# Kernel tuning notes

Measured on AMD Instinct MI355X. Metric: run time of the kernel, lower is better.

The kernel has to match this reference:

```python
import jax, jax.numpy as jnp
import numpy as np

TEMPERATURE = 0.1

def _l2norm(x):
    # F.normalize(dim=1) with eps clamp
    n = jnp.maximum(jnp.linalg.norm(x, axis=1, keepdims=True), 1e-12)
    return x / n

def _retrieval_metric(s):
    # T=1: position of the diagonal element in each row's descending sort.
    order = jnp.argsort(-s, axis=1)            # [N,N] descending argsort
    rankpos = jnp.argsort(order, axis=1)        # inverse permutation: rank of each column
    pos = jnp.diagonal(rankpos)                 # j such that rank[i][j] == i
    posf = pos.astype(s.dtype)
    r1 = jnp.mean((pos < 1).astype(s.dtype))
    r5 = jnp.mean((pos < 5).astype(s.dtype))
    r10 = jnp.mean((pos < 10).astype(s.dtype))
    mr = jnp.mean(posf)
    return r1, r5, r10, mr

def setup_inputs() -> dict:
    key = jax.random.key(0)
    k1, k2, k3, k4 = jax.random.split(key, 4)
    N, C = 4096, 512
    return {
        'v_feat': jax.random.normal(k1, (N, C), dtype=jnp.float32),
        't_feat': jax.random.normal(k2, (N, C), dtype=jnp.float32),
        'p_v': jax.random.normal(k3, (N, C), dtype=jnp.float32),
        'p_t': jax.random.normal(k4, (N, C), dtype=jnp.float32),
    }

def reference(v_feat, t_feat, p_v, p_t):
    vn = _l2norm(v_feat)
    tn = _l2norm(t_feat)
    pvn = _l2norm(p_v)
    ptn = _l2norm(p_t)
    sv = jnp.einsum('nc,mc->nm', vn, ptn) / TEMPERATURE  # [N,N]
    st = jnp.einsum('nc,mc->nm', tn, pvn) / TEMPERATURE  # [N,N]
    # nominator: scalar logsumexp over both diagonals (2N values)
    nominator = jax.nn.logsumexp(jnp.concatenate([jnp.diagonal(sv), jnp.diagonal(st)], axis=0))
    # denominator: per-row logsumexp over concatenated [N,2N]
    denominator = jax.nn.logsumexp(jnp.concatenate([sv, st], axis=1), axis=1)
    loss = jnp.mean(denominator - nominator)
    # metrics (no-grad path in original)
    v_std = jnp.mean(jnp.std(vn, axis=0, ddof=1))
    t_std = jnp.mean(jnp.std(tn, axis=0, ddof=1))
    pv_std = jnp.mean(jnp.std(pvn, axis=0, ddof=1))
    pt_std = jnp.mean(jnp.std(ptn, axis=0, ddof=1))
    sv_raw = jnp.einsum('nc,mc->nm', vn, ptn)
    st_raw = jnp.einsum('nc,mc->nm', tn, pvn)
    v_r1, v_r5, v_r10, v_mr = _retrieval_metric(sv_raw)
    t_r1, t_r5, t_r10, t_mr = _retrieval_metric(st_raw)
    return (loss, v_std, t_std, pv_std, pt_std,
            v_r1, v_r5, v_r10, v_mr,
            t_r1, t_r5, t_r10, t_mr)
```

## Files before the change

### kernel.cpp

```cpp
#include <hip/hip_runtime.h>
#include <hip/hip_bf16.h>

#define N 4096
#define C 512

typedef __attribute__((ext_vector_type(8))) short bf16x8;
typedef __attribute__((ext_vector_type(8))) short s16x8;
typedef __attribute__((ext_vector_type(4))) float f32x4;

__device__ inline float bf2f(__hip_bfloat16 h) { return __bfloat162float(h); }
__device__ inline float bfbits2f(unsigned short b) {
    union { unsigned u; float f; } c; c.u = ((unsigned)b) << 16; return c.f;
}

__device__ inline void gload16(const void* g, void* l) {
    __builtin_amdgcn_global_load_lds(
        (__attribute__((address_space(1))) void*)(g),
        (__attribute__((address_space(3))) void*)(l),
        16, 0, 0);
}

__global__ __launch_bounds__(256) void k_norm_split(
    const float* __restrict__ s0, const float* __restrict__ s1f,
    const float* __restrict__ s2f, const float* __restrict__ s3,
    __hip_bfloat16* __restrict__ ws_hi0, long mat_stride)
{
    const int m = blockIdx.x >> 12;
    const int row = blockIdx.x & 4095;
    const int tid = threadIdx.x;
    const float* src = (m == 0) ? s0 : (m == 1) ? s1f : (m == 2) ? s2f : s3;
    __hip_bfloat16* hi = ws_hi0 + (long)m * mat_stride;
    __hip_bfloat16* lo = hi + (long)N * C;

    const float2* r = (const float2*)(src + (size_t)row * C);
    float2 x = r[tid];
    float ss = x.x * x.x + x.y * x.y;
    for (int o = 1; o < 64; o <<= 1) ss += __shfl_xor(ss, o);
    __shared__ float wsum[4];
    if ((tid & 63) == 0) wsum[tid >> 6] = ss;
    __syncthreads();
    float tot = wsum[0] + wsum[1] + wsum[2] + wsum[3];
    float scale = 1.0f / fmaxf(sqrtf(tot), 1e-12f);
    float y0 = x.x * scale, y1 = x.y * scale;
    __hip_bfloat16 h0 = __float2bfloat16(y0);
    __hip_bfloat16 h1 = __float2bfloat16(y1);
    __hip_bfloat16 l0 = __float2bfloat16(y0 - bf2f(h0));
    __hip_bfloat16 l1 = __float2bfloat16(y1 - bf2f(h1));
    size_t base = (size_t)row * C + 2 * tid;
    hi[base] = h0; hi[base + 1] = h1;
    lo[base] = l0; lo[base + 1] = l1;
}

__global__ __launch_bounds__(256) void k_diag(
    const unsigned short* __restrict__ h0, const unsigned short* __restrict__ l0,
    const unsigned short* __restrict__ h1, const unsigned short* __restrict__ l1,
    const unsigned short* __restrict__ h2, const unsigned short* __restrict__ l2,
    const unsigned short* __restrict__ h3, const unsigned short* __restrict__ l3,
    float* __restrict__ dv, float* __restrict__ dt)
{
    const int lane = threadIdx.x & 63;
    const int w = threadIdx.x >> 6;
    const int row = blockIdx.x * 4 + w;
    const int z = blockIdx.y;
    const unsigned short* ah = z ? h1 : h0;
    const unsigned short* al = z ? l1 : l0;
    const unsigned short* bh = z ? h2 : h3;
    const unsigned short* bl = z ? l2 : l3;
    float* dout = z ? dt : dv;

    size_t base = (size_t)row * C + lane * 8;
    s16x8 xh = *(const s16x8*)(ah + base);
    s16x8 xl = *(const s16x8*)(al + base);
    s16x8 yh = *(const s16x8*)(bh + base);
    s16x8 yl = *(const s16x8*)(bl + base);
    float s = 0.f;
    for (int e = 0; e < 8; e++) {
        float a = bfbits2f((unsigned short)xh[e]);
        float b = bfbits2f((unsigned short)xl[e]);
        float c = bfbits2f((unsigned short)yh[e]);
        float d = bfbits2f((unsigned short)yl[e]);
        s += a * c + a * d + b * c;
    }
    for (int o = 1; o < 64; o <<= 1) s += __shfl_xor(s, o);
    if (lane == 0) dout[row] = s;
}

__global__ __launch_bounds__(256) void k_gemm(
    const __hip_bfloat16* __restrict__ h0, const __hip_bfloat16* __restrict__ l0,
    const __hip_bfloat16* __restrict__ h1, const __hip_bfloat16* __restrict__ l1,
    const __hip_bfloat16* __restrict__ h2, const __hip_bfloat16* __restrict__ l2,
    const __hip_bfloat16* __restrict__ h3, const __hip_bfloat16* __restrict__ l3,
    const float* __restrict__ dv, const float* __restrict__ dt,
    float* __restrict__ pev, float* __restrict__ pet,
    float* __restrict__ pcv, float* __restrict__ pct)
{
    __shared__ __align__(16) __hip_bfloat16 sA[2][128][32];
    __shared__ __align__(16) __hip_bfloat16 sB[2][128][32];
    __shared__ float sdiag[128];
    __shared__ float sred[128][2][2];

    const int z = blockIdx.z;
    const __hip_bfloat16* Ah = z ? h1 : h0;
    const __hip_bfloat16* Al = z ? l1 : l0;
    const __hip_bfloat16* Bh = z ? h2 : h3;
    const __hip_bfloat16* Bl = z ? l2 : l3;
    const float* diag = z ? dt : dv;
    float* pe = z ? pet : pev;
    float* pc = z ? pct : pcv;

    const int tid = threadIdx.x;
    const int lane = tid & 63;
    const int w = tid >> 6;
    const int wy = w >> 1, wx = w & 1;
    const int bm = blockIdx.x * 128;
    const int bn = blockIdx.y * 128;

    if (tid < 128) sdiag[tid] = diag[bm + tid];

    f32x4 acc[4][4];
    for (int i = 0; i < 4; i++)
        for (int j = 0; j < 4; j++)
            acc[i][j] = (f32x4){0.f, 0.f, 0.f, 0.f};

    const int srow = lane >> 2;
    const int scol = (lane & 3) * 8;
    const int fr = lane & 15;
    const int fq = (lane >> 4) * 8;

    for (int k0 = 0; k0 < C; k0 += 32) {
        for (int half = 0; half < 2; half++) {
            int rr = w * 16 + half * 64 + srow;
            size_t ga = (size_t)(bm + rr) * C + k0 + scol;
            size_t gb = (size_t)(bn + rr) * C + k0 + scol;
            gload16(Ah + ga, &sA[0][rr][scol]);
            gload16(Al + ga, &sA[1][rr][scol]);
            gload16(Bh + gb, &sB[0][rr][scol]);
            gload16(Bl + gb, &sB[1][rr][scol]);
        }
        __syncthreads();

        bf16x8 a_h[4], a_l[4], b_h[4], b_l[4];
        for (int i = 0; i < 4; i++) {
            a_h[i] = *(const bf16x8*)&sA[0][wy * 64 + i * 16 + fr][fq];
            a_l[i] = *(const bf16x8*)&sA[1][wy * 64 + i * 16 + fr][fq];
            b_h[i] = *(const bf16x8*)&sB[0][wx * 64 + i * 16 + fr][fq];
            b_l[i] = *(const bf16x8*)&sB[1][wx * 64 + i * 16 + fr][fq];
        }
        for (int i = 0; i < 4; i++)
            for (int j = 0; j < 4; j++) {
                acc[i][j] = __builtin_amdgcn_mfma_f32_16x16x32_bf16(a_h[i], b_h[j], acc[i][j], 0, 0, 0);
                acc[i][j] = __builtin_amdgcn_mfma_f32_16x16x32_bf16(a_h[i], b_l[j], acc[i][j], 0, 0, 0);
                acc[i][j] = __builtin_amdgcn_mfma_f32_16x16x32_bf16(a_l[i], b_h[j], acc[i][j], 0, 0, 0);
            }
        __syncthreads();
    }

    const int quad = lane >> 4;
    for (int i = 0; i < 4; i++) {
        for (int reg = 0; reg < 4; reg++) {
            int rloc = wy * 64 + i * 16 + quad * 4 + reg;
            int grow = bm + rloc;
            float d = sdiag[rloc];
            float e = 0.f, c = 0.f;
            for (int j = 0; j < 4; j++) {
                float s = acc[i][j][reg];
                int gcol = bn + wx * 64 + j * 16 + fr;
                e += __expf(10.f * s - 10.f);
                if (s > d && gcol != grow) c += 1.f;
            }
            for (int o = 1; o < 16; o <<= 1) {
                e += __shfl_xor(e, o);
                c += __shfl_xor(c, o);
            }
            if (fr == 0) { sred[rloc][wx][0] = e; sred[rloc][wx][1] = c; }
        }
    }
    __syncthreads();
    if (tid < 128) {
        size_t idx = (size_t)(bm + tid) * 32 + blockIdx.y;
        pe[idx] = sred[tid][0][0] + sred[tid][1][0];
        pc[idx] = sred[tid][0][1] + sred[tid][1][1];
    }
}

__global__ __launch_bounds__(512) void k_stdp(
    const __hip_bfloat16* __restrict__ ws_hi0, long mat_stride,
    float* __restrict__ s1, float* __restrict__ s2)
{
    const int col = threadIdx.x;
    const int chunk = blockIdx.x;
    const int m = blockIdx.y;
    const __hip_bfloat16* hi = ws_hi0 + (long)m * mat_stride;
    const __hip_bfloat16* lo = hi + (long)N * C;
    float a = 0.f, b = 0.f;
    for (int r = chunk * 64; r < chunk * 64 + 64; r++) {
        float y = bf2f(hi[(size_t)r * C + col]) + bf2f(lo[(size_t)r * C + col]);
        a += y;
        b += y * y;
    }
    size_t idx = ((size_t)m * 64 + chunk) * 512 + col;
    s1[idx] = a;
    s2[idx] = b;
}

__global__ __launch_bounds__(64) void k_rowred(
    const float* __restrict__ dv, const float* __restrict__ dt,
    const float* __restrict__ pev, const float* __restrict__ pet,
    const float* __restrict__ pcv, const float* __restrict__ pct,
    float* __restrict__ partials)
{
    const int lane = threadIdx.x;
    const int row = blockIdx.x * 64 + lane;

    float se = 0.f, pv = 0.f, pt = 0.f;
    for (int cb = 0; cb < 32; cb++) {
        se += pev[(size_t)row * 32 + cb] + pet[(size_t)row * 32 + cb];
        pv += pcv[(size_t)row * 32 + cb];
        pt += pct[(size_t)row * 32 + cb];
    }

    float vals[10];
    vals[0] = logf(se) + 10.f;
    vals[1] = (pv < 0.5f) ? 1.f : 0.f;
    vals[2] = (pv < 4.5f) ? 1.f : 0.f;
    vals[3] = (pv < 9.5f) ? 1.f : 0.f;
    vals[4] = pv;
    vals[5] = (pt < 0.5f) ? 1.f : 0.f;
    vals[6] = (pt < 4.5f) ? 1.f : 0.f;
    vals[7] = (pt < 9.5f) ? 1.f : 0.f;
    vals[8] = pt;
    vals[9] = __expf(10.f * dv[row] - 10.f) + __expf(10.f * dt[row] - 10.f);

    for (int k = 0; k < 10; k++) {
        float v = vals[k];
        for (int o = 1; o < 64; o <<= 1) v += __shfl_xor(v, o);
        if (lane == k) partials[(size_t)blockIdx.x * 10 + k] = v;
    }
}

__global__ __launch_bounds__(64) void k_colstd(
    const float* __restrict__ s1, const float* __restrict__ s2,
    float* __restrict__ stdpart)
{
    const int lane = threadIdx.x;
    const int m = blockIdx.x >> 3;
    const int col = (blockIdx.x & 7) * 64 + lane;
    float a = 0.f, b = 0.f;
    for (int ch = 0; ch < 64; ch++) {
        size_t idx = ((size_t)m * 64 + ch) * 512 + col;
        a += s1[idx];
        b += s2[idx];
    }
    float var = (b - a * a * (1.f / N)) * (1.f / (N - 1));
    float sd = sqrtf(fmaxf(var, 0.f));
    for (int o = 1; o < 64; o <<= 1) sd += __shfl_xor(sd, o);
    if (lane == 0) stdpart[blockIdx.x] = sd;
}

__global__ __launch_bounds__(64) void k_final2(
    const float* __restrict__ partials,
    const float* __restrict__ stdpart,
    float* __restrict__ out)
{
    const int lane = threadIdx.x;
    float v = 0.f;
    if (lane < 10) {
        for (int b = 0; b < 64; b++) v += partials[b * 10 + lane];
    }
    __shared__ float g[10];
    __shared__ float stds[4];
    if (lane < 10) g[lane] = v;
    if (lane < 4) {
        float s = 0.f;
        for (int i = 0; i < 8; i++) s += stdpart[lane * 8 + i];
        stds[lane] = s * (1.f / 512.f);
    }
    __syncthreads();
    if (lane == 0) {
        const float invN = 1.f / N;
        float nominator = logf(g[9]) + 10.f;
        out[0]  = g[0] * invN - nominator;
        out[1]  = stds[0];
        out[2]  = stds[1];
        out[3]  = stds[2];
        out[4]  = stds[3];
        out[5]  = g[1] * invN;
        out[6]  = g[2] * invN;
        out[7]  = g[3] * invN;
        out[8]  = g[4] * invN;
        out[9]  = g[5] * invN;
        out[10] = g[6] * invN;
        out[11] = g[7] * invN;
        out[12] = g[8] * invN;
    }
}

extern "C" void kernel_launch(void* const* d_in, const int* in_sizes, int n_in,
                              void* d_out, int out_size, void* d_ws, size_t ws_size,
                              hipStream_t stream)
{
    char* p = (char*)d_ws;
    const size_t NE = (size_t)N * C;
    const long mat_stride = 2 * NE;
    __hip_bfloat16* hiA[4];
    __hip_bfloat16* loA[4];
    for (int m = 0; m < 4; m++) {
        hiA[m] = (__hip_bfloat16*)p; p += NE * 2;
        loA[m] = (__hip_bfloat16*)p; p += NE * 2;
    }
    float* dv  = (float*)p; p += N * 4;
    float* dt  = (float*)p; p += N * 4;
    float* pev = (float*)p; p += 32 * N * 4;
    float* pet = (float*)p; p += 32 * N * 4;
    float* pcv = (float*)p; p += 32 * N * 4;
    float* pct = (float*)p; p += 32 * N * 4;
    float* s1  = (float*)p; p += 4 * 64 * 512 * 4;
    float* s2  = (float*)p; p += 4 * 64 * 512 * 4;
    float* partials = (float*)p; p += 64 * 10 * 4;
    float* stdpart  = (float*)p; p += 32 * 4;

    k_norm_split<<<dim3(4 * N), 256, 0, stream>>>(
        (const float*)d_in[0], (const float*)d_in[1],
        (const float*)d_in[2], (const float*)d_in[3],
        hiA[0], mat_stride);

    k_diag<<<dim3(N / 4, 2), 256, 0, stream>>>(
        (const unsigned short*)hiA[0], (const unsigned short*)loA[0],
        (const unsigned short*)hiA[1], (const unsigned short*)loA[1],
        (const unsigned short*)hiA[2], (const unsigned short*)loA[2],
        (const unsigned short*)hiA[3], (const unsigned short*)loA[3],
        dv, dt);

    k_gemm<<<dim3(32, 32, 2), 256, 0, stream>>>(
        hiA[0], loA[0], hiA[1], loA[1], hiA[2], loA[2], hiA[3], loA[3],
        dv, dt, pev, pet, pcv, pct);

    k_stdp<<<dim3(64, 4), 512, 0, stream>>>(hiA[0], mat_stride, s1, s2);

    k_rowred<<<dim3(64), 64, 0, stream>>>(dv, dt, pev, pet, pcv, pct, partials);
    k_colstd<<<dim3(32), 64, 0, stream>>>(s1, s2, stdpart);
    k_final2<<<dim3(1), 64, 0, stream>>>(partials, stdpart, (float*)d_out);
}
```

Baseline: 223.5 us.

## Fuse prep kernels, swizzle GEMM LDS layout, merge final reductions via atomic counter

Merges normalization/split, diagonal dot products, and column std statistics into one k_prep launch. Diagonals and column sums are now computed directly from the fp32 inputs, so the bf16 hi/lo buffers are no longer re-read. The GEMM staging gains an XOR swizzle on LDS columns to reduce bank conflicts on fragment reads. The three tail kernels collapse into one k_fin that uses a last-block atomic counter for the final combine. This cuts launch count and memory traffic, at the cost of heavier prep blocks and reliance on threadfence/atomic ordering.

```diff
diff --git a/kernel.cpp b/kernel.cpp
--- a/kernel.cpp
+++ b/kernel.cpp
@@ -20,69 +20,109 @@
         16, 0, 0);
 }
 
-__global__ __launch_bounds__(256) void k_norm_split(
+__global__ __launch_bounds__(256) void k_prep(
     const float* __restrict__ s0, const float* __restrict__ s1f,
     const float* __restrict__ s2f, const float* __restrict__ s3,
-    __hip_bfloat16* __restrict__ ws_hi0, long mat_stride)
+    __hip_bfloat16* __restrict__ ws_hi0, long mat_stride,
+    float* __restrict__ dv, float* __restrict__ dt,
+    float* __restrict__ st1, float* __restrict__ st2,
+    unsigned int* __restrict__ counter)
 {
-    const int m = blockIdx.x >> 12;
-    const int row = blockIdx.x & 4095;
+    __shared__ float sa[4][512];
+    __shared__ float sb[4][512];
+
+    const int b = blockIdx.x;
     const int tid = threadIdx.x;
-    const float* src = (m == 0) ? s0 : (m == 1) ? s1f : (m == 2) ? s2f : s3;
-    __hip_bfloat16* hi = ws_hi0 + (long)m * mat_stride;
-    __hip_bfloat16* lo = hi + (long)N * C;
-
-    const float2* r = (const float2*)(src + (size_t)row * C);
-    float2 x = r[tid];
-    float ss = x.x * x.x + x.y * x.y;
-    for (int o = 1; o < 64; o <<= 1) ss += __shfl_xor(ss, o);
-    __shared__ float wsum[4];
-    if ((tid & 63) == 0) wsum[tid >> 6] = ss;
-    __syncthreads();
-    float tot = wsum[0] + wsum[1] + wsum[2] + wsum[3];
-    float scale = 1.0f / fmaxf(sqrtf(tot), 1e-12f);
-    float y0 = x.x * scale, y1 = x.y * scale;
-    __hip_bfloat16 h0 = __float2bfloat16(y0);
-    __hip_bfloat16 h1 = __float2bfloat16(y1);
-    __hip_bfloat16 l0 = __float2bfloat16(y0 - bf2f(h0));
-    __hip_bfloat16 l1 = __float2bfloat16(y1 - bf2f(h1));
-    size_t base = (size_t)row * C + 2 * tid;
-    hi[base] = h0; hi[base + 1] = h1;
-    lo[base] = l0; lo[base + 1] = l1;
-}
-
-__global__ __launch_bounds__(256) void k_diag(
-    const unsigned short* __restrict__ h0, const unsigned short* __restrict__ l0,
-    const unsigned short* __restrict__ h1, const unsigned short* __restrict__ l1,
-    const unsigned short* __restrict__ h2, const unsigned short* __restrict__ l2,
-    const unsigned short* __restrict__ h3, const unsigned short* __restrict__ l3,
-    float* __restrict__ dv, float* __restrict__ dt)
-{
-    const int lane = threadIdx.x & 63;
-    const int w = threadIdx.x >> 6;
-    const int row = blockIdx.x * 4 + w;
-    const int z = blockIdx.y;
-    const unsigned short* ah = z ? h1 : h0;
-    const unsigned short* al = z ? l1 : l0;
-    const unsigned short* bh = z ? h2 : h3;
-    const unsigned short* bl = z ? l2 : l3;
-    float* dout = z ? dt : dv;
-
-    size_t base = (size_t)row * C + lane * 8;
-    s16x8 xh = *(const s16x8*)(ah + base);
-    s16x8 xl = *(const s16x8*)(al + base);
-    s16x8 yh = *(const s16x8*)(bh + base);
-    s16x8 yl = *(const s16x8*)(bl + base);
-    float s = 0.f;
-    for (int e = 0; e < 8; e++) {
-        float a = bfbits2f((unsigned short)xh[e]);
-        float b = bfbits2f((unsigned short)xl[e]);
-        float c = bfbits2f((unsigned short)yh[e]);
-        float d = bfbits2f((unsigned short)yl[e]);
-        s += a * c + a * d + b * c;
-    }
-    for (int o = 1; o < 64; o <<= 1) s += __shfl_xor(s, o);
-    if (lane == 0) dout[row] = s;
+    const int lane = tid & 63;
+    const int w = tid >> 6;
+
+    if (b == 0 && tid == 0) *counter = 0;
+
+    if (b < 4096) {
+        const int grow = b * 4 + w;
+        const int m = grow >> 12;
+        const int row = grow & 4095;
+        const float* src = (m == 0) ? s0 : (m == 1) ? s1f : (m == 2) ? s2f : s3;
+        __hip_bfloat16* hi = ws_hi0 + (long)m * mat_stride;
+        __hip_bfloat16* lo = hi + (long)N * C;
+
+        const float4* r4 = (const float4*)(src + (size_t)row * C);
+        float4 x0 = r4[lane * 2];
+        float4 x1 = r4[lane * 2 + 1];
+        float ss = x0.x*x0.x + x0.y*x0.y + x0.z*x0.z + x0.w*x0.w
+                 + x1.x*x1.x + x1.y*x1.y + x1.z*x1.z + x1.w*x1.w;
+        for (int o = 1; o < 64; o <<= 1) ss += __shfl_xor(ss, o);
+        float scale = 1.0f / fmaxf(sqrtf(ss), 1e-12f);
+        float y[8] = { x0.x*scale, x0.y*scale, x0.z*scale, x0.w*scale,
+                       x1.x*scale, x1.y*scale, x1.z*scale, x1.w*scale };
+        __hip_bfloat16 hv[8], lv[8];
+        for (int e = 0; e < 8; e++) {
+            hv[e] = __float2bfloat16(y[e]);
+            lv[e] = __float2bfloat16(y[e] - bf2f(hv[e]));
+        }
+        size_t base = (size_t)row * C + lane * 8;
+        *(s16x8*)(hi + base) = *(s16x8*)hv;
+        *(s16x8*)(lo + base) = *(s16x8*)lv;
+    } else if (b < 6144) {
+        const int idx = b - 4096;
+        const int z = idx >> 10;
+        const int row = (idx & 1023) * 4 + w;
+        const float* A = z ? s1f : s0;
+        const float* B = z ? s2f : s3;
+        float* dout = z ? dt : dv;
+
+        const float4* a4 = (const float4*)(A + (size_t)row * C);
+        const float4* b4 = (const float4*)(B + (size_t)row * C);
+        float4 a0 = a4[lane * 2], a1 = a4[lane * 2 + 1];
+        float4 b0 = b4[lane * 2], b1 = b4[lane * 2 + 1];
+        float ssa = a0.x*a0.x + a0.y*a0.y + a0.z*a0.z + a0.w*a0.w
+                  + a1.x*a1.x + a1.y*a1.y + a1.z*a1.z + a1.w*a1.w;
+        float ssb = b0.x*b0.x + b0.y*b0.y + b0.z*b0.z + b0.w*b0.w
+                  + b1.x*b1.x + b1.y*b1.y + b1.z*b1.z + b1.w*b1.w;
+        float dot = a0.x*b0.x + a0.y*b0.y + a0.z*b0.z + a0.w*b0.w
+                  + a1.x*b1.x + a1.y*b1.y + a1.z*b1.z + a1.w*b1.w;
+        for (int o = 1; o < 64; o <<= 1) {
+            ssa += __shfl_xor(ssa, o);
+            ssb += __shfl_xor(ssb, o);
+            dot += __shfl_xor(dot, o);
+        }
+        if (lane == 0)
+            dout[row] = dot / (fmaxf(sqrtf(ssa), 1e-12f) * fmaxf(sqrtf(ssb), 1e-12f));
+    } else {
+        const int idx = b - 6144;
+        const int m = idx >> 5;
+        const int chunk = idx & 31;
+        const float* src = (m == 0) ? s0 : (m == 1) ? s1f : (m == 2) ? s2f : s3;
+        const int slice = w;
+
+        float a[8], q[8];
+        for (int e = 0; e < 8; e++) { a[e] = 0.f; q[e] = 0.f; }
+        const int row0 = chunk * 128 + slice * 32;
+        for (int r = 0; r < 32; r++) {
+            const float4* r4 = (const float4*)(src + (size_t)(row0 + r) * C);
+            float4 x0 = r4[lane * 2];
+            float4 x1 = r4[lane * 2 + 1];
+            float ss = x0.x*x0.x + x0.y*x0.y + x0.z*x0.z + x0.w*x0.w
+                     + x1.x*x1.x + x1.y*x1.y + x1.z*x1.z + x1.w*x1.w;
+            for (int o = 1; o < 64; o <<= 1) ss += __shfl_xor(ss, o);
+            float scale = 1.0f / fmaxf(sqrtf(ss), 1e-12f);
+            float y[8] = { x0.x*scale, x0.y*scale, x0.z*scale, x0.w*scale,
+                           x1.x*scale, x1.y*scale, x1.z*scale, x1.w*scale };
+            for (int e = 0; e < 8; e++) { a[e] += y[e]; q[e] += y[e] * y[e]; }
+        }
+        for (int e = 0; e < 8; e++) {
+            sa[slice][lane * 8 + e] = a[e];
+            sb[slice][lane * 8 + e] = q[e];
+        }
+        __syncthreads();
+        for (int c = tid; c < 512; c += 256) {
+            float A = sa[0][c] + sa[1][c] + sa[2][c] + sa[3][c];
+            float B = sb[0][c] + sb[1][c] + sb[2][c] + sb[3][c];
+            size_t o = ((size_t)m * 32 + chunk) * 512 + c;
+            st1[o] = A;
+            st2[o] = B;
+        }
+    }
 }
 
 __global__ __launch_bounds__(256) void k_gemm(
@@ -123,28 +163,29 @@
             acc[i][j] = (f32x4){0.f, 0.f, 0.f, 0.f};
 
     const int srow = lane >> 2;
-    const int scol = (lane & 3) * 8;
+    const int lcol = (lane & 3) * 8;
+    const int scolg = (((lane & 3) ^ ((lane >> 3) & 3))) * 8;
     const int fr = lane & 15;
-    const int fq = (lane >> 4) * 8;
+    const int pcs = ((lane >> 4) ^ ((fr >> 1) & 3)) * 8;
 
     for (int k0 = 0; k0 < C; k0 += 32) {
         for (int half = 0; half < 2; half++) {
             int rr = w * 16 + half * 64 + srow;
-            size_t ga = (size_t)(bm + rr) * C + k0 + scol;
-            size_t gb = (size_t)(bn + rr) * C + k0 + scol;
-            gload16(Ah + ga, &sA[0][rr][scol]);
-            gload16(Al + ga, &sA[1][rr][scol]);
-            gload16(Bh + gb, &sB[0][rr][scol]);
-            gload16(Bl + gb, &sB[1][rr][scol]);
+            size_t ga = (size_t)(bm + rr) * C + k0 + scolg;
+            size_t gb = (size_t)(bn + rr) * C + k0 + scolg;
+            gload16(Ah + ga, &sA[0][rr][lcol]);
+            gload16(Al + ga, &sA[1][rr][lcol]);
+            gload16(Bh + gb, &sB[0][rr][lcol]);
+            gload16(Bl + gb, &sB[1][rr][lcol]);
         }
         __syncthreads();
 
         bf16x8 a_h[4], a_l[4], b_h[4], b_l[4];
         for (int i = 0; i < 4; i++) {
-            a_h[i] = *(const bf16x8*)&sA[0][wy * 64 + i * 16 + fr][fq];
-            a_l[i] = *(const bf16x8*)&sA[1][wy * 64 + i * 16 + fr][fq];
-            b_h[i] = *(const bf16x8*)&sB[0][wx * 64 + i * 16 + fr][fq];
-            b_l[i] = *(const bf16x8*)&sB[1][wx * 64 + i * 16 + fr][fq];
+            a_h[i] = *(const bf16x8*)&sA[0][wy * 64 + i * 16 + fr][pcs];
+            a_l[i] = *(const bf16x8*)&sA[1][wy * 64 + i * 16 + fr][pcs];
+            b_h[i] = *(const bf16x8*)&sB[0][wx * 64 + i * 16 + fr][pcs];
+            b_l[i] = *(const bf16x8*)&sB[1][wx * 64 + i * 16 + fr][pcs];
         }
         for (int i = 0; i < 4; i++)
             for (int j = 0; j < 4; j++) {
@@ -183,89 +224,75 @@
     }
 }
 
-__global__ __launch_bounds__(512) void k_stdp(
-    const __hip_bfloat16* __restrict__ ws_hi0, long mat_stride,
-    float* __restrict__ s1, float* __restrict__ s2)
-{
-    const int col = threadIdx.x;
-    const int chunk = blockIdx.x;
-    const int m = blockIdx.y;
-    const __hip_bfloat16* hi = ws_hi0 + (long)m * mat_stride;
-    const __hip_bfloat16* lo = hi + (long)N * C;
-    float a = 0.f, b = 0.f;
-    for (int r = chunk * 64; r < chunk * 64 + 64; r++) {
-        float y = bf2f(hi[(size_t)r * C + col]) + bf2f(lo[(size_t)r * C + col]);
-        a += y;
-        b += y * y;
-    }
-    size_t idx = ((size_t)m * 64 + chunk) * 512 + col;
-    s1[idx] = a;
-    s2[idx] = b;
-}
-
-__global__ __launch_bounds__(64) void k_rowred(
+__global__ __launch_bounds__(64) void k_fin(
     const float* __restrict__ dv, const float* __restrict__ dt,
     const float* __restrict__ pev, const float* __restrict__ pet,
     const float* __restrict__ pcv, const float* __restrict__ pct,
-    float* __restrict__ partials)
+    const float* __restrict__ st1, const float* __restrict__ st2,
+    float* __restrict__ partials, float* __restrict__ stdpart,
+    unsigned int* __restrict__ counter, float* __restrict__ out)
 {
+    const int b = blockIdx.x;
     const int lane = threadIdx.x;
-    const int row = blockIdx.x * 64 + lane;
-
-    float se = 0.f, pv = 0.f, pt = 0.f;
-    for (int cb = 0; cb < 32; cb++) {
-        se += pev[(size_t)row * 32 + cb] + pet[(size_t)row * 32 + cb];
-        pv += pcv[(size_t)row * 32 + cb];
-        pt += pct[(size_t)row * 32 + cb];
-    }
-
-    float vals[10];
-    vals[0] = logf(se) + 10.f;
-    vals[1] = (pv < 0.5f) ? 1.f : 0.f;
-    vals[2] = (pv < 4.5f) ? 1.f : 0.f;
-    vals[3] = (pv < 9.5f) ? 1.f : 0.f;
-    vals[4] = pv;
-    vals[5] = (pt < 0.5f) ? 1.f : 0.f;
-    vals[6] = (pt < 4.5f) ? 1.f : 0.f;
-    vals[7] = (pt < 9.5f) ? 1.f : 0.f;
-    vals[8] = pt;
-    vals[9] = __expf(10.f * dv[row] - 10.f) + __expf(10.f * dt[row] - 10.f);
-
-    for (int k = 0; k < 10; k++) {
-        float v = vals[k];
-        for (int o = 1; o < 64; o <<= 1) v += __shfl_xor(v, o);
-        if (lane == k) partials[(size_t)blockIdx.x * 10 + k] = v;
-    }
-}
-
-__global__ __launch_bounds__(64) void k_colstd(
-    const float* __restrict__ s1, const float* __restrict__ s2,
-    float* __restrict__ stdpart)
-{
-    const int lane = threadIdx.x;
-    const int m = blockIdx.x >> 3;
-    const int col = (blockIdx.x & 7) * 64 + lane;
-    float a = 0.f, b = 0.f;
-    for (int ch = 0; ch < 64; ch++) {
-        size_t idx = ((size_t)m * 64 + ch) * 512 + col;
-        a += s1[idx];
-        b += s2[idx];
-    }
-    float var = (b - a * a * (1.f / N)) * (1.f / (N - 1));
-    float sd = sqrtf(fmaxf(var, 0.f));
-    for (int o = 1; o < 64; o <<= 1) sd += __shfl_xor(sd, o);
-    if (lane == 0) stdpart[blockIdx.x] = sd;
-}
-
-__global__ __launch_bounds__(64) void k_final2(
-    const float* __restrict__ partials,
-    const float* __restrict__ stdpart,
-    float* __restrict__ out)
-{
-    const int lane = threadIdx.x;
+
+    if (b < 64) {
+        const int row = b * 64 + lane;
+        float se = 0.f, pv = 0.f, pt = 0.f;
+        const float4* e4v = (const float4*)(pev + (size_t)row * 32);
+        const float4* e4t = (const float4*)(pet + (size_t)row * 32);
+        const float4* c4v = (const float4*)(pcv + (size_t)row * 32);
+        const float4* c4t = (const float4*)(pct + (size_t)row * 32);
+        for (int q = 0; q < 8; q++) {
+            float4 a = e4v[q], bb = e4t[q], c = c4v[q], d = c4t[q];
+            se += a.x + a.y + a.z + a.w + bb.x + bb.y + bb.z + bb.w;
+            pv += c.x + c.y + c.z + c.w;
+            pt += d.x + d.y + d.z + d.w;
+        }
+        float vals[10];
+        vals[0] = logf(se) + 10.f;
+        vals[1] = (pv < 0.5f) ? 1.f : 0.f;
+        vals[2] = (pv < 4.5f) ? 1.f : 0.f;
+        vals[3] = (pv < 9.5f) ? 1.f : 0.f;
+        vals[4] = pv;
+        vals[5] = (pt < 0.5f) ? 1.f : 0.f;
+        vals[6] = (pt < 4.5f) ? 1.f : 0.f;
+        vals[7] = (pt < 9.5f) ? 1.f : 0.f;
+        vals[8] = pt;
+        vals[9] = __expf(10.f * dv[row] - 10.f) + __expf(10.f * dt[row] - 10.f);
+        for (int k = 0; k < 10; k++) {
+            float v = vals[k];
+            for (int o = 1; o < 64; o <<= 1) v += __shfl_xor(v, o);
+            if (lane == k) partials[(size_t)b * 10 + k] = v;
+        }
+    } else {
+        const int idx = b - 64;
+        const int m = idx >> 3;
+        const int col = (idx & 7) * 64 + lane;
+        float a = 0.f, q = 0.f;
+        for (int ch = 0; ch < 32; ch++) {
+            size_t o = ((size_t)m * 32 + ch) * 512 + col;
+            a += st1[o];
+            q += st2[o];
+        }
+        float var = (q - a * a * (1.f / N)) * (1.f / (N - 1));
+        float sd = sqrtf(fmaxf(var, 0.f));
+        for (int o = 1; o < 64; o <<= 1) sd += __shfl_xor(sd, o);
+        if (lane == 0) stdpart[idx] = sd;
+    }
+
+    __syncthreads();
+    __shared__ unsigned int s_old;
+    if (lane == 0) {
+        __threadfence();
+        s_old = atomicAdd(counter, 1u);
+    }
+    __syncthreads();
+    if (s_old != 95) return;
+    __threadfence();
+
     float v = 0.f;
     if (lane < 10) {
-        for (int b = 0; b < 64; b++) v += partials[b * 10 + lane];
+        for (int k = 0; k < 64; k++) v += partials[k * 10 + lane];
     }
     __shared__ float g[10];
     __shared__ float stds[4];
@@ -314,30 +341,22 @@
     float* pet = (float*)p; p += 32 * N * 4;
     float* pcv = (float*)p; p += 32 * N * 4;
     float* pct = (float*)p; p += 32 * N * 4;
-    float* s1  = (float*)p; p += 4 * 64 * 512 * 4;
-    float* s2  = (float*)p; p += 4 * 64 * 512 * 4;
+    float* st1 = (float*)p; p += 4 * 32 * 512 * 4;
+    float* st2 = (float*)p; p += 4 * 32 * 512 * 4;
     float* partials = (float*)p; p += 64 * 10 * 4;
     float* stdpart  = (float*)p; p += 32 * 4;
-
-    k_norm_split<<<dim3(4 * N), 256, 0, stream>>>(
+    unsigned int* counter = (unsigned int*)p; p += 16;
+
+    k_prep<<<dim3(6272), 256, 0, stream>>>(
         (const float*)d_in[0], (const float*)d_in[1],
         (const float*)d_in[2], (const float*)d_in[3],
-        hiA[0], mat_stride);
-
-    k_diag<<<dim3(N / 4, 2), 256, 0, stream>>>(
-        (const unsigned short*)hiA[0], (const unsigned short*)loA[0],
-        (const unsigned short*)hiA[1], (const unsigned short*)loA[1],
-        (const unsigned short*)hiA[2], (const unsigned short*)loA[2],
-        (const unsigned short*)hiA[3], (const unsigned short*)loA[3],
-        dv, dt);
+        hiA[0], mat_stride, dv, dt, st1, st2, counter);
 
     k_gemm<<<dim3(32, 32, 2), 256, 0, stream>>>(
         hiA[0], loA[0], hiA[1], loA[1], hiA[2], loA[2], hiA[3], loA[3],
         dv, dt, pev, pet, pcv, pct);
 
-    k_stdp<<<dim3(64, 4), 512, 0, stream>>>(hiA[0], mat_stride, s1, s2);
-
-    k_rowred<<<dim3(64), 64, 0, stream>>>(dv, dt, pev, pet, pcv, pct, partials);
-    k_colstd<<<dim3(32), 64, 0, stream>>>(s1, s2, stdpart);
-    k_final2<<<dim3(1), 64, 0, stream>>>(partials, stdpart, (float*)d_out);
-}
+    k_fin<<<dim3(96), 64, 0, stream>>>(
+        dv, dt, pev, pet, pcv, pct, st1, st2,
+        partials, stdpart, counter, (float*)d_out);
+}
```

New measurement: 217.0 us. 2.9% less time.
